# Kernel optimization log

Hardware: AMD Instinct MI355X
Metric: run time of the kernel (lower is better)

Reference implementation:

```python
import jax, jax.numpy as jnp
import numpy as np

N_NODES = 50000
N_REL = 3
D_IN = 128
D_OUT = 128
N_EDGES = 600000


def setup_inputs() -> dict:
    key = jax.random.key(0)
    k = jax.random.split(key, 5)
    x = jax.random.normal(k[0], (N_NODES, D_IN), jnp.float32)
    W = jax.random.normal(k[1], (N_REL, D_IN, D_OUT), jnp.float32) / np.sqrt(D_IN)
    b = jax.random.normal(k[2], (N_REL, D_OUT), jnp.float32) * 0.01
    src = jax.random.randint(k[3], (N_REL, N_EDGES), 0, N_NODES, dtype=jnp.int64)
    dst = jax.random.randint(k[4], (N_REL, N_EDGES), 0, N_NODES, dtype=jnp.int64)
    return {"x": x, "W": W, "b": b, "src": src, "dst": dst}


def reference(x, W, b, src, dst):
    n_nodes = x.shape[0]
    # Per-relation linear projection (nn.Linear per etype): [R, N, F_out]
    wh = jnp.einsum('nd,rdf->rnf', x, W) + b[:, None, :]

    def agg_one_rel(wh_r, src_r, dst_r):
        msgs = wh_r[src_r]  # copy_u gather: [E, F_out]
        return jax.ops.segment_sum(msgs, dst_r, num_segments=n_nodes)  # fn.sum

    per_rel = jax.vmap(agg_one_rel)(wh, src, dst)  # [R, N, F_out]
    # multi_update_all cross-reducer 'sum' over edge types
    return per_rel.sum(axis=0)
```

## Files before the change

kernel.cpp:

```cpp
#include <hip/hip_runtime.h>
#include <stdint.h>

#define N_NODES 50000
#define N_REL   3
#define D       128
#define N_EDGES 600000
#define NPAD    50016
#define BK_SHIFT 10
#define NBK     49
#define NCHUNK  512
#define CH_EDGES 1172
#define CH_CAP  64
#define OVF_CAP 8192
#define REG_CAP 20480

typedef unsigned int   uint;
typedef unsigned short ushort_t;
typedef __attribute__((ext_vector_type(8))) short short8v;
typedef __attribute__((ext_vector_type(4))) float f32x4;

__device__ __forceinline__ ushort_t f2bf(float f)
{
    uint u = __float_as_uint(f);
    u += 0x7FFFu + ((u >> 16) & 1u);
    return (ushort_t)(u >> 16);
}
__device__ __forceinline__ float bf_lo(uint u) { return __uint_as_float(u << 16); }
__device__ __forceinline__ float bf_hi(uint u) { return __uint_as_float(u & 0xFFFF0000u); }

__global__ __launch_bounds__(256) void zero_cnt(int* __restrict__ p, int n)
{
    const int i = blockIdx.x * 256 + threadIdx.x;
    if (i < n) p[i] = 0;
}

__global__ __launch_bounds__(256) void cvtW(const float* __restrict__ W,
                                            ushort_t* __restrict__ Wt)
{
    const int idx = blockIdx.x * 256 + threadIdx.x;
    if (idx >= N_REL * D * D) return;
    const int r   = idx >> 14;
    const int rem = idx & 16383;
    const int n   = rem >> 7;
    const int k   = rem & 127;
    Wt[idx] = f2bf(W[r * 16384 + k * 128 + n]);
}

__global__ __launch_bounds__(256, 3) void wh_gemm(
    const float* __restrict__ x, const ushort_t* __restrict__ Wt_all,
    const float* __restrict__ b, ushort_t* __restrict__ wh_all)
{
    __shared__ ushort_t xs[64][136];
    __shared__ ushort_t wt[128][136];

    const int r = blockIdx.y;
    const ushort_t* Wt = Wt_all + (size_t)r * D * D;
    const float* br = b + (size_t)r * D;
    ushort_t* wh = wh_all + (size_t)r * N_NODES * D;

    const int tid  = threadIdx.x;
    const int lane = tid & 63;
    const int w    = tid >> 6;
    const int row0 = blockIdx.x * 64;

    #pragma unroll
    for (int i = 0; i < 8; ++i) {
        const int idx = i * 256 + tid;
        const int rr  = idx >> 5;
        const int c4  = idx & 31;
        const int gr  = row0 + rr;
        float4 v = make_float4(0.f, 0.f, 0.f, 0.f);
        if (gr < N_NODES) v = *(const float4*)(x + (size_t)gr * D + c4 * 4);
        ushort4 o;
        o.x = f2bf(v.x); o.y = f2bf(v.y); o.z = f2bf(v.z); o.w = f2bf(v.w);
        *(ushort4*)&xs[rr][c4 * 4] = o;
    }
    #pragma unroll
    for (int i = 0; i < 8; ++i) {
        const int idx = i * 256 + tid;
        const int n   = idx >> 4;
        const int k8  = idx & 15;
        const uint4 v = *(const uint4*)(Wt + n * D + k8 * 8);
        *(uint4*)&wt[n][k8 * 8] = v;
    }
    __syncthreads();

    const int rl = lane & 15;
    const int kg = lane >> 4;

    f32x4 acc[4][2];
    #pragma unroll
    for (int m = 0; m < 4; ++m)
        #pragma unroll
        for (int n = 0; n < 2; ++n) acc[m][n] = (f32x4){0.f, 0.f, 0.f, 0.f};

    #pragma unroll
    for (int ks = 0; ks < 4; ++ks) {
        short8v a[4], bb[2];
        #pragma unroll
        for (int m = 0; m < 4; ++m)
            a[m] = *(const short8v*)&xs[m * 16 + rl][ks * 32 + kg * 8];
        #pragma unroll
        for (int n = 0; n < 2; ++n)
            bb[n] = *(const short8v*)&wt[w * 32 + n * 16 + rl][ks * 32 + kg * 8];
        #pragma unroll
        for (int m = 0; m < 4; ++m)
            #pragma unroll
            for (int n = 0; n < 2; ++n)
                acc[m][n] = __builtin_amdgcn_mfma_f32_16x16x32_bf16(
                    a[m], bb[n], acc[m][n], 0, 0, 0);
    }

    #pragma unroll
    for (int n = 0; n < 2; ++n) {
        const int col = w * 32 + n * 16 + rl;
        const float bias = br[col];
        #pragma unroll
        for (int m = 0; m < 4; ++m)
            #pragma unroll
            for (int q = 0; q < 4; ++q) {
                const int grow = row0 + m * 16 + kg * 4 + q;
                if (grow < N_NODES)
                    wh[(size_t)grow * D + col] = f2bf(acc[m][n][q] + bias);
            }
    }
}

__global__ __launch_bounds__(256) void bucketA2(const int* __restrict__ src,
                                                const int* __restrict__ dst,
                                                uint* __restrict__ bkt,
                                                int* __restrict__ ccnt,
                                                uint* __restrict__ ovf,
                                                int* __restrict__ ovf_cnt)
{
    __shared__ uint bins[NBK][CH_CAP];
    __shared__ int bcnt[NBK];

    const int r   = blockIdx.y;
    const int ch  = blockIdx.x;
    const int tid = threadIdx.x;

    for (int i = tid; i < NBK; i += 256) bcnt[i] = 0;
    __syncthreads();

    const int* srcr = src + (size_t)r * N_EDGES;
    const int* dstr = dst + (size_t)r * N_EDGES;
    const int e0 = ch * CH_EDGES;
    const int e1 = min(e0 + CH_EDGES, N_EDGES);

    for (int e = e0 + tid; e < e1; e += 256) {
        const uint d = (uint)dstr[e];
        const uint s = (uint)srcr[e];
        const int cb = (int)(d >> BK_SHIFT);
        const uint rec = (d << 16) | s;
        const int lp = atomicAdd(&bcnt[cb], 1);
        if (lp < CH_CAP) {
            bins[cb][lp] = rec;
        } else {
            const int p = atomicAdd(&ovf_cnt[r], 1);
            ovf[(size_t)r * OVF_CAP + p] = rec;
        }
    }
    __syncthreads();

    const int lane = tid & 63, wid = tid >> 6;
    for (int bin = wid; bin < NBK; bin += 4) {
        const int n = min(bcnt[bin], CH_CAP);
        if (lane == 0) ccnt[(r * NBK + bin) * NCHUNK + ch] = n;
        if (n == 0) continue;
        uint* dp = bkt + ((size_t)(r * NBK + bin) * NCHUNK + ch) * CH_CAP;
        for (int i = lane; i < n; i += 64) dp[i] = bins[bin][i];
    }
}

__global__ __launch_bounds__(1024) void placeB2(const uint* __restrict__ bkt,
                                                const int* __restrict__ ccnt,
                                                const uint* __restrict__ ovf,
                                                const int* __restrict__ ovf_cnt,
                                                int* __restrict__ off,
                                                int* __restrict__ deg,
                                                int* __restrict__ srt)
{
    __shared__ int hcnt[1024];
    __shared__ int pcur[1024];
    __shared__ int ccl[NCHUNK];
    __shared__ int wtot[16], wexc[16];

    const int bx        = blockIdx.x;
    const int r         = blockIdx.y;
    const int region    = r * NBK + bx;
    const size_t rbase  = (size_t)region * REG_CAP;
    const int node_base = bx << BK_SHIFT;
    const int tid       = threadIdx.x;
    const int lane      = tid & 63;
    const int wid       = tid >> 6;

    hcnt[tid] = 0;
    for (int i = tid; i < NCHUNK; i += 1024) ccl[i] = ccnt[region * NCHUNK + i];
    __syncthreads();

    const uint* bb  = bkt + (size_t)region * (NCHUNK * CH_CAP);
    const int   nov = ovf_cnt[r];
    const uint* ovr = ovf + (size_t)r * OVF_CAP;

    for (int sidx = tid; sidx < NCHUNK * CH_CAP; sidx += 1024) {
        if ((sidx & 63) < ccl[sidx >> 6])
            atomicAdd(&hcnt[(bb[sidx] >> 16) & 1023], 1);
    }
    for (int j = tid; j < nov; j += 1024) {
        const uint d = ovr[j] >> 16;
        if ((int)(d >> BK_SHIFT) == bx) atomicAdd(&hcnt[d & 1023], 1);
    }
    __syncthreads();

    const int orig = hcnt[tid];
    int v = orig;
    #pragma unroll
    for (int s = 1; s < 64; s <<= 1) {
        const int t = __shfl_up(v, s, 64);
        if (lane >= s) v += t;
    }
    if (lane == 63) wtot[wid] = v;
    __syncthreads();
    if (tid == 0) {
        int run = 0;
        #pragma unroll
        for (int w = 0; w < 16; ++w) { const int t = wtot[w]; wexc[w] = run; run += t; }
    }
    __syncthreads();
    const int excl = wexc[wid] + (v - orig);

    const int node = node_base + tid;
    if (node < N_NODES) {
        off[r * NPAD + node] = (int)rbase + excl;
        deg[r * NPAD + node] = orig;
    }
    pcur[tid] = excl;
    __syncthreads();

    for (int sidx = tid; sidx < NCHUNK * CH_CAP; sidx += 1024) {
        if ((sidx & 63) < ccl[sidx >> 6]) {
            const uint rec = bb[sidx];
            const int p = atomicAdd(&pcur[(rec >> 16) & 1023], 1);
            srt[rbase + p] = (int)(rec & 0xFFFFu);
        }
    }
    for (int j = tid; j < nov; j += 1024) {
        const uint rec = ovr[j];
        const uint d = rec >> 16;
        if ((int)(d >> BK_SHIFT) == bx) {
            const int p = atomicAdd(&pcur[d & 1023], 1);
            srt[rbase + p] = (int)(rec & 0xFFFFu);
        }
    }
}

__global__ __launch_bounds__(256) void aggregate(const ushort_t* __restrict__ wh_all,
                                                 const int* __restrict__ off,
                                                 const int* __restrict__ deg,
                                                 const int* __restrict__ srt,
                                                 float* __restrict__ out)
{
    const int g    = (blockIdx.x * 256 + threadIdx.x) >> 4;
    const int lane = threadIdx.x & 15;
    if (g >= N_NODES) return;

    float acc[8];
    #pragma unroll
    for (int j = 0; j < 8; ++j) acc[j] = 0.0f;

    for (int r = 0; r < N_REL; ++r) {
        const ushort_t* wh = wh_all + (size_t)r * N_NODES * D;
        const int e0 = off[r * NPAD + g];
        const int e1 = e0 + deg[r * NPAD + g];
        int i = e0;
        for (; i + 2 <= e1; i += 2) {
            const int s0 = srt[i];
            const int s1 = srt[i + 1];
            const uint4 v0 = *(const uint4*)(wh + (size_t)s0 * D + lane * 8);
            const uint4 v1 = *(const uint4*)(wh + (size_t)s1 * D + lane * 8);
            acc[0] += bf_lo(v0.x); acc[1] += bf_hi(v0.x);
            acc[2] += bf_lo(v0.y); acc[3] += bf_hi(v0.y);
            acc[4] += bf_lo(v0.z); acc[5] += bf_hi(v0.z);
            acc[6] += bf_lo(v0.w); acc[7] += bf_hi(v0.w);
            acc[0] += bf_lo(v1.x); acc[1] += bf_hi(v1.x);
            acc[2] += bf_lo(v1.y); acc[3] += bf_hi(v1.y);
            acc[4] += bf_lo(v1.z); acc[5] += bf_hi(v1.z);
            acc[6] += bf_lo(v1.w); acc[7] += bf_hi(v1.w);
        }
        if (i < e1) {
            const int s0 = srt[i];
            const uint4 v0 = *(const uint4*)(wh + (size_t)s0 * D + lane * 8);
            acc[0] += bf_lo(v0.x); acc[1] += bf_hi(v0.x);
            acc[2] += bf_lo(v0.y); acc[3] += bf_hi(v0.y);
            acc[4] += bf_lo(v0.z); acc[5] += bf_hi(v0.z);
            acc[6] += bf_lo(v0.w); acc[7] += bf_hi(v0.w);
        }
    }

    float* o = out + (size_t)g * D + lane * 8;
    *(float4*)(o + 0) = make_float4(acc[0], acc[1], acc[2], acc[3]);
    *(float4*)(o + 4) = make_float4(acc[4], acc[5], acc[6], acc[7]);
}

extern "C" void kernel_launch(void* const* d_in, const int* in_sizes, int n_in,
                              void* d_out, int out_size, void* d_ws, size_t ws_size,
                              hipStream_t stream)
{
    const float* x   = (const float*)d_in[0];
    const float* W   = (const float*)d_in[1];
    const float* b   = (const float*)d_in[2];
    const int*   src = (const int*)d_in[3];
    const int*   dst = (const int*)d_in[4];
    float* out = (float*)d_out;

    const int gemm_gx = (N_NODES + 63) / 64;
    const int agg_gx  = (N_NODES * 16 + 255) / 256;
    const int L       = N_REL * NPAD;
    const int NREG    = N_REL * NBK;

    char* base    = (char*)d_ws;
    ushort_t* wh  = (ushort_t*)base;
    int* off      = (int*)(base + (size_t)N_REL * N_NODES * D * 2);
    int* deg      = off + L;
    int* ovf_cnt  = deg + L;
    uint* ovf     = (uint*)(ovf_cnt + 16);
    int* ccnt     = (int*)(ovf + (size_t)N_REL * OVF_CAP);
    uint* bkt     = (uint*)(ccnt + NREG * NCHUNK);
    int*  srt     = (int*)(bkt + (size_t)NREG * NCHUNK * CH_CAP);
    ushort_t* Wt  = (ushort_t*)(srt + (size_t)NREG * REG_CAP);

    cvtW<<<(N_REL * D * D + 255) / 256, 256, 0, stream>>>(W, Wt);
    wh_gemm<<<dim3(gemm_gx, N_REL), 256, 0, stream>>>(x, Wt, b, wh);
    zero_cnt<<<1, 256, 0, stream>>>(ovf_cnt, 16);
    bucketA2<<<dim3(NCHUNK, N_REL), 256, 0, stream>>>(src, dst, bkt, ccnt, ovf, ovf_cnt);
    placeB2<<<dim3(NBK, N_REL), 1024, 0, stream>>>(bkt, ccnt, ovf, ovf_cnt, off, deg, srt);
    aggregate<<<agg_gx, 256, 0, stream>>>(wh, off, deg, srt, out);
}
```

Before: 218.0 us.

## Use finer node buckets with smaller placement blocks and unroll aggregation gather by four

Buckets now cover 256 destination nodes instead of 1024, so the placement kernel launches 196x3 blocks of 256 threads rather than 49x3 blocks of 1024, which spreads the counting-sort work across more CUs. Each chunk's records are walked by a half-wave up to its real count, so capacity slots past the count are not scanned. The aggregation loop now issues four independent row gathers per iteration to raise memory-level parallelism. The tradeoff is that per-region capacity (4096) and per-chunk capacity (32) are tighter, which leans on the overflow path and fixed caps for skewed degree distributions.

New measurement: 221.2 us. Within noise of the previous version (+1.5%).

```diff
diff --git a/kernel.cpp b/kernel.cpp
--- a/kernel.cpp
+++ b/kernel.cpp
@@ -6,13 +6,13 @@
 #define D       128
 #define N_EDGES 600000
 #define NPAD    50016
-#define BK_SHIFT 10
-#define NBK     49
-#define NCHUNK  512
-#define CH_EDGES 1172
-#define CH_CAP  64
+#define BK_SHIFT 8
+#define NBK     196
+#define NCHUNK  256
+#define CH_EDGES 2344
+#define CH_CAP  32
 #define OVF_CAP 8192
-#define REG_CAP 20480
+#define REG_CAP 4096
 
 typedef unsigned int   uint;
 typedef unsigned short ushort_t;
@@ -173,18 +173,18 @@
     }
 }
 
-__global__ __launch_bounds__(1024) void placeB2(const uint* __restrict__ bkt,
-                                                const int* __restrict__ ccnt,
-                                                const uint* __restrict__ ovf,
-                                                const int* __restrict__ ovf_cnt,
-                                                int* __restrict__ off,
-                                                int* __restrict__ deg,
-                                                int* __restrict__ srt)
-{
-    __shared__ int hcnt[1024];
-    __shared__ int pcur[1024];
+__global__ __launch_bounds__(256) void placeB2(const uint* __restrict__ bkt,
+                                               const int* __restrict__ ccnt,
+                                               const uint* __restrict__ ovf,
+                                               const int* __restrict__ ovf_cnt,
+                                               int* __restrict__ off,
+                                               int* __restrict__ deg,
+                                               int* __restrict__ srt)
+{
+    __shared__ int hcnt[256];
+    __shared__ int pcur[256];
     __shared__ int ccl[NCHUNK];
-    __shared__ int wtot[16], wexc[16];
+    __shared__ int wtot[4], wexc[4];
 
     const int bx        = blockIdx.x;
     const int r         = blockIdx.y;
@@ -194,22 +194,25 @@
     const int tid       = threadIdx.x;
     const int lane      = tid & 63;
     const int wid       = tid >> 6;
+    const int hw        = tid >> 5;
+    const int l32       = tid & 31;
 
     hcnt[tid] = 0;
-    for (int i = tid; i < NCHUNK; i += 1024) ccl[i] = ccnt[region * NCHUNK + i];
+    ccl[tid] = ccnt[region * NCHUNK + tid];
     __syncthreads();
 
     const uint* bb  = bkt + (size_t)region * (NCHUNK * CH_CAP);
     const int   nov = ovf_cnt[r];
     const uint* ovr = ovf + (size_t)r * OVF_CAP;
 
-    for (int sidx = tid; sidx < NCHUNK * CH_CAP; sidx += 1024) {
-        if ((sidx & 63) < ccl[sidx >> 6])
-            atomicAdd(&hcnt[(bb[sidx] >> 16) & 1023], 1);
-    }
-    for (int j = tid; j < nov; j += 1024) {
+    for (int ch = hw; ch < NCHUNK; ch += 8) {
+        const int n = ccl[ch];
+        for (int i = l32; i < n; i += 32)
+            atomicAdd(&hcnt[(bb[ch * CH_CAP + i] >> 16) & 255], 1);
+    }
+    for (int j = tid; j < nov; j += 256) {
         const uint d = ovr[j] >> 16;
-        if ((int)(d >> BK_SHIFT) == bx) atomicAdd(&hcnt[d & 1023], 1);
+        if ((int)(d >> BK_SHIFT) == bx) atomicAdd(&hcnt[d & 255], 1);
     }
     __syncthreads();
 
@@ -225,7 +228,7 @@
     if (tid == 0) {
         int run = 0;
         #pragma unroll
-        for (int w = 0; w < 16; ++w) { const int t = wtot[w]; wexc[w] = run; run += t; }
+        for (int w = 0; w < 4; ++w) { const int t = wtot[w]; wexc[w] = run; run += t; }
     }
     __syncthreads();
     const int excl = wexc[wid] + (v - orig);
@@ -238,18 +241,19 @@
     pcur[tid] = excl;
     __syncthreads();
 
-    for (int sidx = tid; sidx < NCHUNK * CH_CAP; sidx += 1024) {
-        if ((sidx & 63) < ccl[sidx >> 6]) {
-            const uint rec = bb[sidx];
-            const int p = atomicAdd(&pcur[(rec >> 16) & 1023], 1);
+    for (int ch = hw; ch < NCHUNK; ch += 8) {
+        const int n = ccl[ch];
+        for (int i = l32; i < n; i += 32) {
+            const uint rec = bb[ch * CH_CAP + i];
+            const int p = atomicAdd(&pcur[(rec >> 16) & 255], 1);
             srt[rbase + p] = (int)(rec & 0xFFFFu);
         }
     }
-    for (int j = tid; j < nov; j += 1024) {
+    for (int j = tid; j < nov; j += 256) {
         const uint rec = ovr[j];
         const uint d = rec >> 16;
         if ((int)(d >> BK_SHIFT) == bx) {
-            const int p = atomicAdd(&pcur[d & 1023], 1);
+            const int p = atomicAdd(&pcur[d & 255], 1);
             srt[rbase + p] = (int)(rec & 0xFFFFu);
         }
     }
@@ -274,11 +278,15 @@
         const int e0 = off[r * NPAD + g];
         const int e1 = e0 + deg[r * NPAD + g];
         int i = e0;
-        for (; i + 2 <= e1; i += 2) {
-            const int s0 = srt[i];
+        for (; i + 4 <= e1; i += 4) {
+            const int s0 = srt[i + 0];
             const int s1 = srt[i + 1];
+            const int s2 = srt[i + 2];
+            const int s3 = srt[i + 3];
             const uint4 v0 = *(const uint4*)(wh + (size_t)s0 * D + lane * 8);
             const uint4 v1 = *(const uint4*)(wh + (size_t)s1 * D + lane * 8);
+            const uint4 v2 = *(const uint4*)(wh + (size_t)s2 * D + lane * 8);
+            const uint4 v3 = *(const uint4*)(wh + (size_t)s3 * D + lane * 8);
             acc[0] += bf_lo(v0.x); acc[1] += bf_hi(v0.x);
             acc[2] += bf_lo(v0.y); acc[3] += bf_hi(v0.y);
             acc[4] += bf_lo(v0.z); acc[5] += bf_hi(v0.z);
@@ -287,8 +295,16 @@
             acc[2] += bf_lo(v1.y); acc[3] += bf_hi(v1.y);
             acc[4] += bf_lo(v1.z); acc[5] += bf_hi(v1.z);
             acc[6] += bf_lo(v1.w); acc[7] += bf_hi(v1.w);
-        }
-        if (i < e1) {
+            acc[0] += bf_lo(v2.x); acc[1] += bf_hi(v2.x);
+            acc[2] += bf_lo(v2.y); acc[3] += bf_hi(v2.y);
+            acc[4] += bf_lo(v2.z); acc[5] += bf_hi(v2.z);
+            acc[6] += bf_lo(v2.w); acc[7] += bf_hi(v2.w);
+            acc[0] += bf_lo(v3.x); acc[1] += bf_hi(v3.x);
+            acc[2] += bf_lo(v3.y); acc[3] += bf_hi(v3.y);
+            acc[4] += bf_lo(v3.z); acc[5] += bf_hi(v3.z);
+            acc[6] += bf_lo(v3.w); acc[7] += bf_hi(v3.w);
+        }
+        for (; i < e1; ++i) {
             const int s0 = srt[i];
             const uint4 v0 = *(const uint4*)(wh + (size_t)s0 * D + lane * 8);
             acc[0] += bf_lo(v0.x); acc[1] += bf_hi(v0.x);
@@ -334,6 +350,6 @@
     wh_gemm<<<dim3(gemm_gx, N_REL), 256, 0, stream>>>(x, Wt, b, wh);
     zero_cnt<<<1, 256, 0, stream>>>(ovf_cnt, 16);
     bucketA2<<<dim3(NCHUNK, N_REL), 256, 0, stream>>>(src, dst, bkt, ccnt, ovf, ovf_cnt);
-    placeB2<<<dim3(NBK, N_REL), 1024, 0, stream>>>(bkt, ccnt, ovf, ovf_cnt, off, deg, srt);
+    placeB2<<<dim3(NBK, N_REL), 256, 0, stream>>>(bkt, ccnt, ovf, ovf_cnt, off, deg, srt);
     aggregate<<<agg_gx, 256, 0, stream>>>(wh, off, deg, srt, out);
 }
```
